# Kernel tuning notes

Hardware: AMD Instinct MI355X
Metric: run time of the kernel (lower is better)

## Reference

```python
import jax, jax.numpy as jnp
import numpy as np

N, C, X, H = 50000, 8, 256, 256

def setup_inputs() -> dict:
    key = jax.random.key(0)
    k1, k2, k3, k4, k5, k6 = jax.random.split(key, 6)
    child_h = jax.random.normal(k1, (N, C, X), dtype=jnp.float32)
    parent_h = jax.random.normal(k2, (N, X), dtype=jnp.float32)
    u = lambda k, s: jax.random.uniform(k, s, jnp.float32, -0.1, 0.1)
    return {
        "child_h": child_h,
        "parent_h": parent_h,
        "W_left": u(k3, (X, H)),
        "W_right": u(k4, (X, H)),
        "W_top": u(k5, (X, H)),
        "b_conv": u(k6, (1, H)),
    }

def reference(child_h, parent_h, W_left, W_right, W_top, b_conv):
    # Positional continuous-binary-tree weights over C children:
    #   left_w[i]  = (C-1-i)/(C-1),  right_w[i] = i/(C-1)
    C_ = child_h.shape[1]
    i = jnp.arange(C_, dtype=child_h.dtype)
    left_w = (C_ - 1 - i) / (C_ - 1)   # [C]
    right_w = i / (C_ - 1)             # [C]
    # sum_i lw_i*(h_i @ W_l) + rw_i*(h_i @ W_r) == (sum_i lw_i h_i) @ W_l + (sum_i rw_i h_i) @ W_r
    s_left = jnp.einsum("ncx,c->nx", child_h, left_w)    # [N, X]
    s_right = jnp.einsum("ncx,c->nx", child_h, right_w)  # [N, X]
    children_state = s_left @ W_left + s_right @ W_right  # [N, H]
    return jax.nn.relu(children_state + parent_h @ W_top + b_conv)
```

## Files before the change

### kernel.cpp

```cpp
#include <hip/hip_runtime.h>
#include <hip/hip_bf16.h>

#define NROWS 50000
#define CDIM 8
#define XDIM 256
#define HDIM 256

typedef __attribute__((ext_vector_type(8))) short bf16x8;
typedef __attribute__((ext_vector_type(4))) float f32x4;

__device__ __forceinline__ unsigned short f2bf_rne(float f) {
    unsigned int u = __builtin_bit_cast(unsigned int, f);
    u += 0x7fffu + ((u >> 16) & 1u);
    return (unsigned short)(u >> 16);
}

__device__ __forceinline__ bf16x8 pack8(const f32x4 a, const f32x4 b) {
    bf16x8 r;
    r[0] = (short)f2bf_rne(a[0]);
    r[1] = (short)f2bf_rne(a[1]);
    r[2] = (short)f2bf_rne(a[2]);
    r[3] = (short)f2bf_rne(a[3]);
    r[4] = (short)f2bf_rne(b[0]);
    r[5] = (short)f2bf_rne(b[1]);
    r[6] = (short)f2bf_rne(b[2]);
    r[7] = (short)f2bf_rne(b[3]);
    return r;
}

__global__ __launch_bounds__(256) void pack_weights(
        const float* __restrict__ Wl, const float* __restrict__ Wr,
        const float* __restrict__ Wt, bf16x8* __restrict__ wp) {
    int t = blockIdx.x * 256 + threadIdx.x;
    int lane = t & 63;
    int tile = t >> 6;
    int ht  = tile & 15;
    int sx  = tile >> 4;
    int xc  = sx & 7;
    int seg = sx >> 3;
    const float* __restrict__ W = (seg == 0) ? Wl : (seg == 1) ? Wr : Wt;
    int x0 = xc * 32 + (lane >> 4) * 8;
    int h  = ht * 16 + (lane & 15);
    bf16x8 frag;
#pragma unroll
    for (int j = 0; j < 8; ++j)
        frag[j] = (short)f2bf_rne(W[(size_t)(x0 + j) * HDIM + h]);
    wp[t] = frag;
}

__global__ __launch_bounds__(256) void tbcnn_main(
        const float* __restrict__ child, const float* __restrict__ parent,
        const bf16x8* __restrict__ wp, const float* __restrict__ bias,
        float* __restrict__ out) {
    const int wave = threadIdx.x >> 6;
    const int lane = threadIdx.x & 63;
    const int wtask = blockIdx.x * 4 + wave;
    const int row0 = wtask * 16;
    if (row0 >= NROWS) return;

    const int rmod = lane & 15;
    const int quad = lane >> 4;
    const int row  = row0 + rmod;

    const float* __restrict__ chrow = child  + (size_t)row * (CDIM * XDIM);
    const float* __restrict__ prow  = parent + (size_t)row * XDIM;

    const float lwt[8] = {7.f/7.f, 6.f/7.f, 5.f/7.f, 4.f/7.f, 3.f/7.f, 2.f/7.f, 1.f/7.f, 0.f/7.f};
    const float rwt[8] = {0.f/7.f, 1.f/7.f, 2.f/7.f, 3.f/7.f, 4.f/7.f, 5.f/7.f, 6.f/7.f, 7.f/7.f};

    f32x4 acc[16];
#pragma unroll
    for (int t = 0; t < 16; ++t) acc[t] = (f32x4){0.f, 0.f, 0.f, 0.f};

#pragma unroll 1
    for (int xc = 0; xc < 8; ++xc) {
        const int x0 = xc * 32 + quad * 8;

        f32x4 sl0 = (f32x4){0.f,0.f,0.f,0.f}, sl1 = (f32x4){0.f,0.f,0.f,0.f};
        f32x4 sr0 = (f32x4){0.f,0.f,0.f,0.f}, sr1 = (f32x4){0.f,0.f,0.f,0.f};
#pragma unroll
        for (int c = 0; c < CDIM; ++c) {
            const f32x4* p = (const f32x4*)(chrow + (size_t)c * XDIM + x0);
            f32x4 a = p[0];
            f32x4 b = p[1];
            sl0 += a * lwt[c];  sl1 += b * lwt[c];
            sr0 += a * rwt[c];  sr1 += b * rwt[c];
        }
        const f32x4* pp = (const f32x4*)(prow + x0);
        f32x4 p0 = pp[0];
        f32x4 p1 = pp[1];

        bf16x8 fL = pack8(sl0, sl1);
        bf16x8 fR = pack8(sr0, sr1);
        bf16x8 fP = pack8(p0, p1);

        const bf16x8* wL = wp + ((size_t)((0 * 8 + xc) * 16)) * 64 + lane;
        const bf16x8* wR = wp + ((size_t)((1 * 8 + xc) * 16)) * 64 + lane;
        const bf16x8* wT = wp + ((size_t)((2 * 8 + xc) * 16)) * 64 + lane;
#pragma unroll
        for (int ht = 0; ht < 16; ++ht)
            acc[ht] = __builtin_amdgcn_mfma_f32_16x16x32_bf16(wL[ht * 64], fL, acc[ht], 0, 0, 0);
#pragma unroll
        for (int ht = 0; ht < 16; ++ht)
            acc[ht] = __builtin_amdgcn_mfma_f32_16x16x32_bf16(wR[ht * 64], fR, acc[ht], 0, 0, 0);
#pragma unroll
        for (int ht = 0; ht < 16; ++ht)
            acc[ht] = __builtin_amdgcn_mfma_f32_16x16x32_bf16(wT[ht * 64], fP, acc[ht], 0, 0, 0);
    }

    float* __restrict__ orow = out + (size_t)row * HDIM;
#pragma unroll
    for (int ht = 0; ht < 16; ++ht) {
        const int h = ht * 16 + quad * 4;
        f32x4 b4 = *(const f32x4*)(bias + h);
        f32x4 v = acc[ht];
        v[0] = fmaxf(v[0] + b4[0], 0.f);
        v[1] = fmaxf(v[1] + b4[1], 0.f);
        v[2] = fmaxf(v[2] + b4[2], 0.f);
        v[3] = fmaxf(v[3] + b4[3], 0.f);
        *(f32x4*)(orow + h) = v;
    }
}

__global__ __launch_bounds__(256) void tbcnn_fallback(
        const float* __restrict__ child, const float* __restrict__ parent,
        const float* __restrict__ Wl, const float* __restrict__ Wr,
        const float* __restrict__ Wt, const float* __restrict__ bias,
        float* __restrict__ out) {
    __shared__ float sl[XDIM], sr[XDIM], sp[XDIM];
    const int n = blockIdx.x;
    const int h = threadIdx.x;
    const float lwt[8] = {7.f/7.f, 6.f/7.f, 5.f/7.f, 4.f/7.f, 3.f/7.f, 2.f/7.f, 1.f/7.f, 0.f/7.f};
    const float* ch = child + (size_t)n * (CDIM * XDIM);
    float al = 0.f, ar = 0.f;
#pragma unroll
    for (int c = 0; c < CDIM; ++c) {
        float v = ch[c * XDIM + h];
        al += lwt[c] * v;
        ar += (1.f - lwt[c]) * v;
    }
    ar = 0.f;
    const float rwt[8] = {0.f/7.f, 1.f/7.f, 2.f/7.f, 3.f/7.f, 4.f/7.f, 5.f/7.f, 6.f/7.f, 7.f/7.f};
#pragma unroll
    for (int c = 0; c < CDIM; ++c) ar += rwt[c] * ch[c * XDIM + h];
    sl[h] = al; sr[h] = ar; sp[h] = parent[(size_t)n * XDIM + h];
    __syncthreads();
    float a = bias[h];
    for (int x = 0; x < XDIM; ++x)
        a += sl[x] * Wl[(size_t)x * HDIM + h] + sr[x] * Wr[(size_t)x * HDIM + h]
           + sp[x] * Wt[(size_t)x * HDIM + h];
    out[(size_t)n * HDIM + h] = fmaxf(a, 0.f);
}

extern "C" void kernel_launch(void* const* d_in, const int* in_sizes, int n_in,
                              void* d_out, int out_size, void* d_ws, size_t ws_size,
                              hipStream_t stream) {
    const float* child  = (const float*)d_in[0];
    const float* parent = (const float*)d_in[1];
    const float* Wl     = (const float*)d_in[2];
    const float* Wr     = (const float*)d_in[3];
    const float* Wt     = (const float*)d_in[4];
    const float* bias   = (const float*)d_in[5];
    float* out = (float*)d_out;

    const size_t wp_bytes = (size_t)3 * XDIM * HDIM * sizeof(unsigned short);
    if (ws_size >= wp_bytes) {
        bf16x8* wp = (bf16x8*)d_ws;
        pack_weights<<<96, 256, 0, stream>>>(Wl, Wr, Wt, wp);
        const int n_wtasks = NROWS / 16;
        const int n_blocks = (n_wtasks + 3) / 4;
        tbcnn_main<<<n_blocks, 256, 0, stream>>>(child, parent, wp, bias, out);
    } else {
        tbcnn_fallback<<<NROWS, 256, 0, stream>>>(child, parent, Wl, Wr, Wt, bias, out);
    }
}
```

Before: 656.2 us.

## Split child reduction into coalesced pre-pass writing bf16 activations before GEMM

Adds a reduce_convert kernel that streams child and parent with coalesced per-row reads, computes the left/right weighted sums, and stores them plus parent as bf16 in workspace. The GEMM kernel then loads ready bf16 fragments instead of doing strided fp32 loads and conversions in its inner loop. This aims to improve memory access efficiency and separate bandwidth-bound and MFMA-bound phases, at the cost of extra intermediate traffic, an additional launch and a larger workspace requirement; the previous fused kernel is kept as a fallback.

```diff
diff --git a/kernel.cpp b/kernel.cpp
--- a/kernel.cpp
+++ b/kernel.cpp
@@ -7,12 +7,22 @@
 #define HDIM 256
 
 typedef __attribute__((ext_vector_type(8))) short bf16x8;
+typedef __attribute__((ext_vector_type(4))) short bf16x4;
 typedef __attribute__((ext_vector_type(4))) float f32x4;
 
 __device__ __forceinline__ unsigned short f2bf_rne(float f) {
     unsigned int u = __builtin_bit_cast(unsigned int, f);
     u += 0x7fffu + ((u >> 16) & 1u);
     return (unsigned short)(u >> 16);
+}
+
+__device__ __forceinline__ bf16x4 pack4(const f32x4 a) {
+    bf16x4 r;
+    r[0] = (short)f2bf_rne(a[0]);
+    r[1] = (short)f2bf_rne(a[1]);
+    r[2] = (short)f2bf_rne(a[2]);
+    r[3] = (short)f2bf_rne(a[3]);
+    return r;
 }
 
 __device__ __forceinline__ bf16x8 pack8(const f32x4 a, const f32x4 b) {
@@ -48,10 +58,42 @@
     wp[t] = frag;
 }
 
-__global__ __launch_bounds__(256) void tbcnn_main(
+__global__ __launch_bounds__(256) void reduce_convert(
         const float* __restrict__ child, const float* __restrict__ parent,
-        const bf16x8* __restrict__ wp, const float* __restrict__ bias,
-        float* __restrict__ out) {
+        bf16x4* __restrict__ slb, bf16x4* __restrict__ srb,
+        bf16x4* __restrict__ pb) {
+    const int tid = blockIdx.x * 256 + threadIdx.x;
+    const int row = tid >> 6;
+    const int xi  = tid & 63;
+
+    const float lwt[8] = {7.f/7.f, 6.f/7.f, 5.f/7.f, 4.f/7.f, 3.f/7.f, 2.f/7.f, 1.f/7.f, 0.f/7.f};
+    const float rwt[8] = {0.f/7.f, 1.f/7.f, 2.f/7.f, 3.f/7.f, 4.f/7.f, 5.f/7.f, 6.f/7.f, 7.f/7.f};
+
+    const float* __restrict__ ch = child + (size_t)row * (CDIM * XDIM) + xi * 4;
+
+    f32x4 cv[CDIM];
+#pragma unroll
+    for (int c = 0; c < CDIM; ++c)
+        cv[c] = *(const f32x4*)(ch + (size_t)c * XDIM);
+
+    f32x4 sl = (f32x4){0.f,0.f,0.f,0.f}, sr = (f32x4){0.f,0.f,0.f,0.f};
+#pragma unroll
+    for (int c = 0; c < CDIM; ++c) {
+        sl += cv[c] * lwt[c];
+        sr += cv[c] * rwt[c];
+    }
+    f32x4 pv = *(const f32x4*)(parent + (size_t)row * XDIM + xi * 4);
+
+    const size_t o = (size_t)row * 64 + xi;
+    slb[o] = pack4(sl);
+    srb[o] = pack4(sr);
+    pb[o]  = pack4(pv);
+}
+
+__global__ __launch_bounds__(256) void tbcnn_gemm(
+        const short* __restrict__ slb, const short* __restrict__ srb,
+        const short* __restrict__ pb, const bf16x8* __restrict__ wp,
+        const float* __restrict__ bias, float* __restrict__ out) {
     const int wave = threadIdx.x >> 6;
     const int lane = threadIdx.x & 63;
     const int wtask = blockIdx.x * 4 + wave;
@@ -62,41 +104,25 @@
     const int quad = lane >> 4;
     const int row  = row0 + rmod;
 
-    const float* __restrict__ chrow = child  + (size_t)row * (CDIM * XDIM);
-    const float* __restrict__ prow  = parent + (size_t)row * XDIM;
-
-    const float lwt[8] = {7.f/7.f, 6.f/7.f, 5.f/7.f, 4.f/7.f, 3.f/7.f, 2.f/7.f, 1.f/7.f, 0.f/7.f};
-    const float rwt[8] = {0.f/7.f, 1.f/7.f, 2.f/7.f, 3.f/7.f, 4.f/7.f, 5.f/7.f, 6.f/7.f, 7.f/7.f};
+    const short* __restrict__ slrow = slb + (size_t)row * XDIM + quad * 8;
+    const short* __restrict__ srrow = srb + (size_t)row * XDIM + quad * 8;
+    const short* __restrict__ prow  = pb  + (size_t)row * XDIM + quad * 8;
 
     f32x4 acc[16];
 #pragma unroll
     for (int t = 0; t < 16; ++t) acc[t] = (f32x4){0.f, 0.f, 0.f, 0.f};
+
+    const bf16x8* __restrict__ wbase = wp + lane;
 
 #pragma unroll 1
     for (int xc = 0; xc < 8; ++xc) {
-        const int x0 = xc * 32 + quad * 8;
-
-        f32x4 sl0 = (f32x4){0.f,0.f,0.f,0.f}, sl1 = (f32x4){0.f,0.f,0.f,0.f};
-        f32x4 sr0 = (f32x4){0.f,0.f,0.f,0.f}, sr1 = (f32x4){0.f,0.f,0.f,0.f};
-#pragma unroll
-        for (int c = 0; c < CDIM; ++c) {
-            const f32x4* p = (const f32x4*)(chrow + (size_t)c * XDIM + x0);
-            f32x4 a = p[0];
-            f32x4 b = p[1];
-            sl0 += a * lwt[c];  sl1 += b * lwt[c];
-            sr0 += a * rwt[c];  sr1 += b * rwt[c];
-        }
-        const f32x4* pp = (const f32x4*)(prow + x0);
-        f32x4 p0 = pp[0];
-        f32x4 p1 = pp[1];
-
-        bf16x8 fL = pack8(sl0, sl1);
-        bf16x8 fR = pack8(sr0, sr1);
-        bf16x8 fP = pack8(p0, p1);
-
-        const bf16x8* wL = wp + ((size_t)((0 * 8 + xc) * 16)) * 64 + lane;
-        const bf16x8* wR = wp + ((size_t)((1 * 8 + xc) * 16)) * 64 + lane;
-        const bf16x8* wT = wp + ((size_t)((2 * 8 + xc) * 16)) * 64 + lane;
+        bf16x8 fL = *(const bf16x8*)(slrow + xc * 32);
+        bf16x8 fR = *(const bf16x8*)(srrow + xc * 32);
+        bf16x8 fP = *(const bf16x8*)(prow  + xc * 32);
+
+        const bf16x8* wL = wbase + (size_t)((0 * 8 + xc) * 16) * 64;
+        const bf16x8* wR = wbase + (size_t)((1 * 8 + xc) * 16) * 64;
+        const bf16x8* wT = wbase + (size_t)((2 * 8 + xc) * 16) * 64;
 #pragma unroll
         for (int ht = 0; ht < 16; ++ht)
             acc[ht] = __builtin_amdgcn_mfma_f32_16x16x32_bf16(wL[ht * 64], fL, acc[ht], 0, 0, 0);
@@ -122,6 +148,76 @@
     }
 }
 
+__global__ __launch_bounds__(256) void tbcnn_fused(
+        const float* __restrict__ child, const float* __restrict__ parent,
+        const bf16x8* __restrict__ wp, const float* __restrict__ bias,
+        float* __restrict__ out) {
+    const int wave = threadIdx.x >> 6;
+    const int lane = threadIdx.x & 63;
+    const int wtask = blockIdx.x * 4 + wave;
+    const int row0 = wtask * 16;
+    if (row0 >= NROWS) return;
+
+    const int rmod = lane & 15;
+    const int quad = lane >> 4;
+    const int row  = row0 + rmod;
+
+    const float* __restrict__ chrow = child  + (size_t)row * (CDIM * XDIM);
+    const float* __restrict__ prow  = parent + (size_t)row * XDIM;
+
+    const float lwt[8] = {7.f/7.f, 6.f/7.f, 5.f/7.f, 4.f/7.f, 3.f/7.f, 2.f/7.f, 1.f/7.f, 0.f/7.f};
+    const float rwt[8] = {0.f/7.f, 1.f/7.f, 2.f/7.f, 3.f/7.f, 4.f/7.f, 5.f/7.f, 6.f/7.f, 7.f/7.f};
+
+    f32x4 acc[16];
+#pragma unroll
+    for (int t = 0; t < 16; ++t) acc[t] = (f32x4){0.f, 0.f, 0.f, 0.f};
+
+#pragma unroll 1
+    for (int xc = 0; xc < 8; ++xc) {
+        const int x0 = xc * 32 + quad * 8;
+        f32x4 sl0 = (f32x4){0.f,0.f,0.f,0.f}, sl1 = (f32x4){0.f,0.f,0.f,0.f};
+        f32x4 sr0 = (f32x4){0.f,0.f,0.f,0.f}, sr1 = (f32x4){0.f,0.f,0.f,0.f};
+#pragma unroll
+        for (int c = 0; c < CDIM; ++c) {
+            const f32x4* p = (const f32x4*)(chrow + (size_t)c * XDIM + x0);
+            f32x4 a = p[0];
+            f32x4 b = p[1];
+            sl0 += a * lwt[c];  sl1 += b * lwt[c];
+            sr0 += a * rwt[c];  sr1 += b * rwt[c];
+        }
+        const f32x4* pp = (const f32x4*)(prow + x0);
+        bf16x8 fL = pack8(sl0, sl1);
+        bf16x8 fR = pack8(sr0, sr1);
+        bf16x8 fP = pack8(pp[0], pp[1]);
+
+        const bf16x8* wL = wp + ((size_t)((0 * 8 + xc) * 16)) * 64 + lane;
+        const bf16x8* wR = wp + ((size_t)((1 * 8 + xc) * 16)) * 64 + lane;
+        const bf16x8* wT = wp + ((size_t)((2 * 8 + xc) * 16)) * 64 + lane;
+#pragma unroll
+        for (int ht = 0; ht < 16; ++ht)
+            acc[ht] = __builtin_amdgcn_mfma_f32_16x16x32_bf16(wL[ht * 64], fL, acc[ht], 0, 0, 0);
+#pragma unroll
+        for (int ht = 0; ht < 16; ++ht)
+            acc[ht] = __builtin_amdgcn_mfma_f32_16x16x32_bf16(wR[ht * 64], fR, acc[ht], 0, 0, 0);
+#pragma unroll
+        for (int ht = 0; ht < 16; ++ht)
+            acc[ht] = __builtin_amdgcn_mfma_f32_16x16x32_bf16(wT[ht * 64], fP, acc[ht], 0, 0, 0);
+    }
+
+    float* __restrict__ orow = out + (size_t)row * HDIM;
+#pragma unroll
+    for (int ht = 0; ht < 16; ++ht) {
+        const int h = ht * 16 + quad * 4;
+        f32x4 b4 = *(const f32x4*)(bias + h);
+        f32x4 v = acc[ht];
+        v[0] = fmaxf(v[0] + b4[0], 0.f);
+        v[1] = fmaxf(v[1] + b4[1], 0.f);
+        v[2] = fmaxf(v[2] + b4[2], 0.f);
+        v[3] = fmaxf(v[3] + b4[3], 0.f);
+        *(f32x4*)(orow + h) = v;
+    }
+}
+
 __global__ __launch_bounds__(256) void tbcnn_fallback(
         const float* __restrict__ child, const float* __restrict__ parent,
         const float* __restrict__ Wl, const float* __restrict__ Wr,
@@ -131,18 +227,15 @@
     const int n = blockIdx.x;
     const int h = threadIdx.x;
     const float lwt[8] = {7.f/7.f, 6.f/7.f, 5.f/7.f, 4.f/7.f, 3.f/7.f, 2.f/7.f, 1.f/7.f, 0.f/7.f};
+    const float rwt[8] = {0.f/7.f, 1.f/7.f, 2.f/7.f, 3.f/7.f, 4.f/7.f, 5.f/7.f, 6.f/7.f, 7.f/7.f};
     const float* ch = child + (size_t)n * (CDIM * XDIM);
     float al = 0.f, ar = 0.f;
 #pragma unroll
     for (int c = 0; c < CDIM; ++c) {
         float v = ch[c * XDIM + h];
         al += lwt[c] * v;
-        ar += (1.f - lwt[c]) * v;
-    }
-    ar = 0.f;
-    const float rwt[8] = {0.f/7.f, 1.f/7.f, 2.f/7.f, 3.f/7.f, 4.f/7.f, 5.f/7.f, 6.f/7.f, 7.f/7.f};
-#pragma unroll
-    for (int c = 0; c < CDIM; ++c) ar += rwt[c] * ch[c * XDIM + h];
+        ar += rwt[c] * v;
+    }
     sl[h] = al; sr[h] = ar; sp[h] = parent[(size_t)n * XDIM + h];
     __syncthreads();
     float a = bias[h];
@@ -163,13 +256,27 @@
     const float* bias   = (const float*)d_in[5];
     float* out = (float*)d_out;
 
-    const size_t wp_bytes = (size_t)3 * XDIM * HDIM * sizeof(unsigned short);
-    if (ws_size >= wp_bytes) {
+    const size_t wp_bytes  = (size_t)3 * XDIM * HDIM * sizeof(unsigned short);
+    const size_t act_bytes = (size_t)NROWS * XDIM * sizeof(unsigned short);
+    const size_t split_bytes = wp_bytes + 3 * act_bytes;
+
+    if (ws_size >= split_bytes) {
+        char* ws = (char*)d_ws;
+        bf16x8* wp  = (bf16x8*)ws;
+        bf16x4* slb = (bf16x4*)(ws + wp_bytes);
+        bf16x4* srb = (bf16x4*)(ws + wp_bytes + act_bytes);
+        bf16x4* pb  = (bf16x4*)(ws + wp_bytes + 2 * act_bytes);
+
+        pack_weights<<<96, 256, 0, stream>>>(Wl, Wr, Wt, wp);
+        reduce_convert<<<(NROWS * 64) / 256, 256, 0, stream>>>(child, parent, slb, srb, pb);
+        const int n_blocks = (NROWS / 16 + 3) / 4;
+        tbcnn_gemm<<<n_blocks, 256, 0, stream>>>((const short*)slb, (const short*)srb,
+                                                 (const short*)pb, wp, bias, out);
+    } else if (ws_size >= wp_bytes) {
         bf16x8* wp = (bf16x8*)d_ws;
         pack_weights<<<96, 256, 0, stream>>>(Wl, Wr, Wt, wp);
-        const int n_wtasks = NROWS / 16;
-        const int n_blocks = (n_wtasks + 3) / 4;
-        tbcnn_main<<<n_blocks, 256, 0, stream>>>(child, parent, wp, bias, out);
+        const int n_blocks = (NROWS / 16 + 3) / 4;
+        tbcnn_fused<<<n_blocks, 256, 0, stream>>>(child, parent, wp, bias, out);
     } else {
         tbcnn_fallback<<<NROWS, 256, 0, stream>>>(child, parent, Wl, Wr, Wt, bias, out);
     }
```

Measured after the change: 710.0 us. +8.2%, slower.
